# Performance work log

Measured on AMD Instinct MI355X. Metric: run time of the kernel, lower is better.

Reference implementation:

```python
import jax, jax.numpy as jnp
import numpy as np

B, S, D, H = 128, 1024, 512, 512


def setup_inputs() -> dict:
    key = jax.random.key(0)
    ks = jax.random.split(key, 8)
    return {
        "input": jax.random.normal(ks[0], (B, D), jnp.float32),
        "context": jax.random.normal(ks[1], (B, S, D), jnp.float32),
        "mask": jax.random.randint(ks[2], (B, S), 0, 2).astype(bool),
        "W_in": jax.random.normal(ks[3], (H, D), jnp.float32) * (1.0 / np.sqrt(D)),
        "b_in": jax.random.normal(ks[4], (H,), jnp.float32) * 0.01,
        "W_ctx": jax.random.normal(ks[5], (H, D), jnp.float32) * (1.0 / np.sqrt(D)),
        "b_ctx": jax.random.normal(ks[6], (H,), jnp.float32) * 0.01,
        "V": jax.random.uniform(ks[7], (H,), jnp.float32, -1.0, 1.0),
    }


def reference(input, context, mask, W_in, b_in, W_ctx, b_ctx, V):
    # inp: [B, H] -> broadcast over S (torch: unsqueeze(2).expand)
    inp = input @ W_in.T + b_in
    # 1x1 Conv1d over permuted context == per-position linear: [B, H, S]
    ctx = jnp.einsum('bsd,hd->bhs', context, W_ctx) + b_ctx[None, :, None]
    # additive (Bahdanau) score: V . tanh(inp + ctx) over H -> [B, S]
    att = jnp.einsum('h,bhs->bs', V, jnp.tanh(inp[:, :, None] + ctx))
    att = jnp.where(mask, -jnp.inf, att)
    alpha = jax.nn.softmax(att, axis=-1)  # [B, S]
    # weighted sum of projected context: [B, H]
    hidden_state = jnp.einsum('bhs,bs->bh', ctx, alpha)
    return (hidden_state, alpha)
```

## Files before the change

### kernel.cpp

```cpp
#include <hip/hip_runtime.h>
#include <math.h>

#define B_ 128
#define S_ 1024
#define D_ 512
#define H_ 512

typedef _Float16 f16x4 __attribute__((ext_vector_type(4)));
typedef _Float16 f16x8 __attribute__((ext_vector_type(8)));
typedef float    f32x4 __attribute__((ext_vector_type(4)));

__global__ void zero_k(float* __restrict__ p, int n) {
    int i = blockIdx.x * 256 + threadIdx.x;
    if (i < n) p[i] = 0.f;
}

__global__ __launch_bounds__(256) void linear_k(const float* __restrict__ X,
                                                const float* __restrict__ W,
                                                const float* __restrict__ bias,
                                                float* __restrict__ out) {
    int idx = blockIdx.x * 256 + threadIdx.x;
    int b = idx >> 9;
    int h = idx & 511;
    const float4* x = (const float4*)(X + (size_t)b * D_);
    const float4* w = (const float4*)(W + (size_t)h * D_);
    float s = 0.f;
#pragma unroll 8
    for (int k = 0; k < D_ / 4; ++k) {
        float4 xv = x[k], wv = w[k];
        s = fmaf(xv.x, wv.x, s);
        s = fmaf(xv.y, wv.y, s);
        s = fmaf(xv.z, wv.z, s);
        s = fmaf(xv.w, wv.w, s);
    }
    out[idx] = s + bias[h];
}

__device__ inline f16x4 cvt4(float4 v) {
    f16x4 r;
    r[0] = (_Float16)v.x; r[1] = (_Float16)v.y;
    r[2] = (_Float16)v.z; r[3] = (_Float16)v.w;
    return r;
}

__device__ inline float fast_tanh(float x) {
    float e = __expf(2.f * x);
    return 1.f - 2.f / (e + 1.f);
}

__global__ __launch_bounds__(256) void score_mfma(const float* __restrict__ ctx,
                                                  const float* __restrict__ Wc,
                                                  const float* __restrict__ bc,
                                                  const float* __restrict__ Vv,
                                                  const float* __restrict__ inp,
                                                  float* __restrict__ att) {
    __shared__ __align__(16) _Float16 Ah[128][40];
    __shared__ __align__(16) _Float16 Bh[128][40];
    __shared__ float red[8][128];

    const int tid = threadIdx.x;
    const int h0 = blockIdx.x * 128;
    const int s0 = blockIdx.y * 128;
    const int b  = blockIdx.z;

    const int rb  = tid >> 3;
    const int grp = tid & 7;

    const int wave = tid >> 6;
    const int lane = tid & 63;
    const int wm = wave >> 1, wn = wave & 1;
    const int l15 = lane & 15, quad = lane >> 4;

    const float* Abase = Wc  + (size_t)(h0 + rb) * D_ + grp * 4;
    const float* Bbase = ctx + ((size_t)b * S_ + s0 + rb) * D_ + grp * 4;

    f32x4 acc[4][4];
#pragma unroll
    for (int mi = 0; mi < 4; ++mi)
#pragma unroll
        for (int ni = 0; ni < 4; ++ni) acc[mi][ni] = (f32x4){0.f, 0.f, 0.f, 0.f};

    float4 ra[4], rbv[4];
#pragma unroll
    for (int i = 0; i < 4; ++i) {
        ra[i]  = *(const float4*)(Abase + (size_t)(32 * i) * D_);
        rbv[i] = *(const float4*)(Bbase + (size_t)(32 * i) * D_);
    }

    for (int k0 = 0; k0 < D_; k0 += 32) {
        __syncthreads();
#pragma unroll
        for (int i = 0; i < 4; ++i) {
            const int row = rb + 32 * i;
            *(f16x4*)&Ah[row][grp * 4] = cvt4(ra[i]);
            *(f16x4*)&Bh[row][grp * 4] = cvt4(rbv[i]);
        }
        __syncthreads();
        if (k0 + 32 < D_) {
#pragma unroll
            for (int i = 0; i < 4; ++i) {
                ra[i]  = *(const float4*)(Abase + (size_t)(32 * i) * D_ + k0 + 32);
                rbv[i] = *(const float4*)(Bbase + (size_t)(32 * i) * D_ + k0 + 32);
            }
        }
        f16x8 bhf[4];
#pragma unroll
        for (int ni = 0; ni < 4; ++ni)
            bhf[ni] = *(const f16x8*)&Bh[wn * 64 + ni * 16 + l15][quad * 8];
#pragma unroll
        for (int mi = 0; mi < 4; ++mi) {
            f16x8 ah = *(const f16x8*)&Ah[wm * 64 + mi * 16 + l15][quad * 8];
#pragma unroll
            for (int ni = 0; ni < 4; ++ni)
                acc[mi][ni] = __builtin_amdgcn_mfma_f32_16x16x32_f16(ah, bhf[ni], acc[mi][ni], 0, 0, 0);
        }
    }

    float p[4] = {0.f, 0.f, 0.f, 0.f};
#pragma unroll
    for (int mi = 0; mi < 4; ++mi) {
#pragma unroll
        for (int r = 0; r < 4; ++r) {
            const int h = h0 + wm * 64 + mi * 16 + quad * 4 + r;
            const float c  = inp[(size_t)b * H_ + h] + bc[h];
            const float vh = Vv[h];
#pragma unroll
            for (int ni = 0; ni < 4; ++ni)
                p[ni] = fmaf(vh, fast_tanh(c + acc[mi][ni][r]), p[ni]);
        }
    }
    const int cid = wm * 4 + quad;
#pragma unroll
    for (int ni = 0; ni < 4; ++ni)
        red[cid][wn * 64 + ni * 16 + l15] = p[ni];
    __syncthreads();
    if (tid < 128) {
        float s = 0.f;
#pragma unroll
        for (int g = 0; g < 8; ++g) s += red[g][tid];
        atomicAdd(att + (size_t)b * S_ + s0 + tid, s);
    }
}

__global__ __launch_bounds__(256) void softmax_k(const float* __restrict__ att,
                                                 const int* __restrict__ mask,
                                                 float* __restrict__ alpha) {
    const int b = blockIdx.x;
    const int t = threadIdx.x;
    __shared__ float sm[256];
    float v[4];
    float mx = -INFINITY;
#pragma unroll
    for (int i = 0; i < 4; ++i) {
        int s = t + i * 256;
        float a = att[(size_t)b * S_ + s];
        int mk = mask[(size_t)b * S_ + s];
        v[i] = mk ? -INFINITY : a;
        mx = fmaxf(mx, v[i]);
    }
    sm[t] = mx;
    __syncthreads();
    for (int off = 128; off > 0; off >>= 1) {
        if (t < off) sm[t] = fmaxf(sm[t], sm[t + off]);
        __syncthreads();
    }
    mx = sm[0];
    __syncthreads();
    float e[4];
    float sum = 0.f;
#pragma unroll
    for (int i = 0; i < 4; ++i) {
        e[i] = expf(v[i] - mx);
        sum += e[i];
    }
    sm[t] = sum;
    __syncthreads();
    for (int off = 128; off > 0; off >>= 1) {
        if (t < off) sm[t] += sm[t + off];
        __syncthreads();
    }
    float inv = 1.f / sm[0];
#pragma unroll
    for (int i = 0; i < 4; ++i) alpha[(size_t)b * S_ + t + i * 256] = e[i] * inv;
}

__global__ __launch_bounds__(256) void cbar_k(const float* __restrict__ ctx,
                                              const float* __restrict__ alpha,
                                              float* __restrict__ cbar) {
    const int b = blockIdx.y;
    const int s0 = blockIdx.x * 128;
    const int t = threadIdx.x;
    const int c4 = t & 127;
    const int sh = t >> 7;
    __shared__ float al[128];
    __shared__ float4 red[128];
    if (t < 128) al[t] = alpha[(size_t)b * S_ + s0 + t];
    __syncthreads();
    const float4* base = (const float4*)(ctx + ((size_t)b * S_ + s0) * D_);
    float4 c = {0.f, 0.f, 0.f, 0.f};
#pragma unroll 4
    for (int s = sh; s < 128; s += 2) {
        float a = al[s];
        float4 x = base[(size_t)s * (D_ / 4) + c4];
        c.x = fmaf(a, x.x, c.x);
        c.y = fmaf(a, x.y, c.y);
        c.z = fmaf(a, x.z, c.z);
        c.w = fmaf(a, x.w, c.w);
    }
    if (sh == 1) red[c4] = c;
    __syncthreads();
    if (sh == 0) {
        float4 o = red[c4];
        float* dst = cbar + (size_t)b * D_ + c4 * 4;
        atomicAdd(dst + 0, c.x + o.x);
        atomicAdd(dst + 1, c.y + o.y);
        atomicAdd(dst + 2, c.z + o.z);
        atomicAdd(dst + 3, c.w + o.w);
    }
}

extern "C" void kernel_launch(void* const* d_in, const int* in_sizes, int n_in,
                              void* d_out, int out_size, void* d_ws, size_t ws_size,
                              hipStream_t stream) {
    const float* input = (const float*)d_in[0];
    const float* ctx   = (const float*)d_in[1];
    const int*   mask  = (const int*)d_in[2];
    const float* W_in  = (const float*)d_in[3];
    const float* b_in  = (const float*)d_in[4];
    const float* W_ctx = (const float*)d_in[5];
    const float* b_ctx = (const float*)d_in[6];
    const float* V     = (const float*)d_in[7];

    float* hidden = (float*)d_out;
    float* alpha  = (float*)d_out + B_ * H_;

    float* inp  = (float*)d_ws;
    float* att  = inp + B_ * H_;
    float* cbar = att + B_ * S_;

    int nz = B_ * S_ + B_ * D_;
    zero_k<<<(nz + 255) / 256, 256, 0, stream>>>(att, nz);

    linear_k<<<(B_ * H_) / 256, 256, 0, stream>>>(input, W_in, b_in, inp);

    dim3 g2(H_ / 128, S_ / 128, B_);
    score_mfma<<<g2, 256, 0, stream>>>(ctx, W_ctx, b_ctx, V, inp, att);

    softmax_k<<<B_, 256, 0, stream>>>(att, mask, alpha);

    dim3 g4(S_ / 128, B_);
    cbar_k<<<g4, 256, 0, stream>>>(ctx, alpha, cbar);

    linear_k<<<(B_ * H_) / 256, 256, 0, stream>>>(cbar, W_ctx, b_ctx, hidden);
}
```

Baseline: 586.8 us.

## Async-copy context tiles into swizzled LDS and preconvert W_ctx to fp16

```diff
diff --git a/kernel.cpp b/kernel.cpp
--- a/kernel.cpp
+++ b/kernel.cpp
@@ -10,9 +10,30 @@
 typedef _Float16 f16x8 __attribute__((ext_vector_type(8)));
 typedef float    f32x4 __attribute__((ext_vector_type(4)));
 
+typedef __attribute__((address_space(3))) uint32_t lds_u32_t;
+typedef const __attribute__((address_space(1))) uint32_t glb_u32_t;
+
+__device__ __forceinline__ void async_copy16(const void* gsrc, void* ldst) {
+    __builtin_amdgcn_global_load_lds((glb_u32_t*)gsrc, (lds_u32_t*)ldst, 16, 0, 0);
+}
+
 __global__ void zero_k(float* __restrict__ p, int n) {
     int i = blockIdx.x * 256 + threadIdx.x;
     if (i < n) p[i] = 0.f;
+}
+
+__device__ inline f16x4 cvt4(float4 v) {
+    f16x4 r;
+    r[0] = (_Float16)v.x; r[1] = (_Float16)v.y;
+    r[2] = (_Float16)v.z; r[3] = (_Float16)v.w;
+    return r;
+}
+
+__global__ __launch_bounds__(256) void w16_k(const float* __restrict__ W,
+                                             _Float16* __restrict__ out) {
+    int i = blockIdx.x * 256 + threadIdx.x;
+    float4 v = ((const float4*)W)[i];
+    *(f16x4*)(out + 4 * (size_t)i) = cvt4(v);
 }
 
 __global__ __launch_bounds__(256) void linear_k(const float* __restrict__ X,
@@ -36,43 +57,38 @@
     out[idx] = s + bias[h];
 }
 
-__device__ inline f16x4 cvt4(float4 v) {
-    f16x4 r;
-    r[0] = (_Float16)v.x; r[1] = (_Float16)v.y;
-    r[2] = (_Float16)v.z; r[3] = (_Float16)v.w;
-    return r;
-}
-
 __device__ inline float fast_tanh(float x) {
     float e = __expf(2.f * x);
     return 1.f - 2.f / (e + 1.f);
 }
 
 __global__ __launch_bounds__(256) void score_mfma(const float* __restrict__ ctx,
-                                                  const float* __restrict__ Wc,
+                                                  const _Float16* __restrict__ W16,
                                                   const float* __restrict__ bc,
                                                   const float* __restrict__ Vv,
                                                   const float* __restrict__ inp,
                                                   float* __restrict__ att) {
-    __shared__ __align__(16) _Float16 Ah[128][40];
-    __shared__ __align__(16) _Float16 Bh[128][40];
+    __shared__ __align__(16) float Bs[2][4096];
     __shared__ float red[8][128];
 
     const int tid = threadIdx.x;
-    const int h0 = blockIdx.x * 128;
-    const int s0 = blockIdx.y * 128;
-    const int b  = blockIdx.z;
-
-    const int rb  = tid >> 3;
-    const int grp = tid & 7;
+    const int f   = blockIdx.x;
+    const int xcd = f & 7;
+    const int hb  = (f >> 3) & 3;
+    const int g   = (f >> 5) * 8 + xcd;
+    const int h0  = hb * 128;
+    const int s0  = (g & 7) * 128;
+    const int b   = g >> 3;
 
     const int wave = tid >> 6;
     const int lane = tid & 63;
     const int wm = wave >> 1, wn = wave & 1;
     const int l15 = lane & 15, quad = lane >> 4;
 
-    const float* Abase = Wc  + (size_t)(h0 + rb) * D_ + grp * 4;
-    const float* Bbase = ctx + ((size_t)b * S_ + s0 + rb) * D_ + grp * 4;
+    const int lrow  = lane >> 3;
+    const int lslot = lane & 7;
+    const int gk    = lslot ^ lrow;
+    const float* bsrc = ctx + ((size_t)b * S_ + s0 + 32 * wave + lrow) * D_ + gk * 4;
 
     f32x4 acc[4][4];
 #pragma unroll
@@ -80,40 +96,52 @@
 #pragma unroll
         for (int ni = 0; ni < 4; ++ni) acc[mi][ni] = (f32x4){0.f, 0.f, 0.f, 0.f};
 
-    float4 ra[4], rbv[4];
-#pragma unroll
-    for (int i = 0; i < 4; ++i) {
-        ra[i]  = *(const float4*)(Abase + (size_t)(32 * i) * D_);
-        rbv[i] = *(const float4*)(Bbase + (size_t)(32 * i) * D_);
-    }
-
-    for (int k0 = 0; k0 < D_; k0 += 32) {
+    const _Float16* Afrag = W16 + (size_t)(h0 + wm * 64 + l15) * D_ + quad * 8;
+
+#pragma unroll
+    for (int it = 0; it < 4; ++it)
+        async_copy16(bsrc + (size_t)it * 8 * D_, &Bs[0][wave * 1024 + it * 256]);
+    f16x8 af[4], afn[4];
+#pragma unroll
+    for (int mi = 0; mi < 4; ++mi)
+        af[mi] = *(const f16x8*)(Afrag + (size_t)mi * 16 * D_);
+    __syncthreads();
+
+    for (int ks = 0; ks < 16; ++ks) {
+        const int buf = ks & 1;
+        if (ks < 15) {
+            const float* sb = bsrc + (ks + 1) * 32;
+#pragma unroll
+            for (int it = 0; it < 4; ++it)
+                async_copy16(sb + (size_t)it * 8 * D_, &Bs[buf ^ 1][wave * 1024 + it * 256]);
+#pragma unroll
+            for (int mi = 0; mi < 4; ++mi)
+                afn[mi] = *(const f16x8*)(Afrag + (size_t)mi * 16 * D_ + (ks + 1) * 32);
+        }
+        f16x8 bf[4];
+#pragma unroll
+        for (int ni = 0; ni < 4; ++ni) {
+            const int r = wn * 64 + ni * 16 + l15;
+            const int rr = r & 7;
+            const int base = (r >> 3) * 256 + rr * 32;
+            const int s1 = (2 * quad) ^ rr;
+            f32x4 u = *(const f32x4*)&Bs[buf][base + s1 * 4];
+            f32x4 v = *(const f32x4*)&Bs[buf][base + (s1 ^ 1) * 4];
+            f16x8 h;
+            h[0] = (_Float16)u[0]; h[1] = (_Float16)u[1];
+            h[2] = (_Float16)u[2]; h[3] = (_Float16)u[3];
+            h[4] = (_Float16)v[0]; h[5] = (_Float16)v[1];
+            h[6] = (_Float16)v[2]; h[7] = (_Float16)v[3];
+            bf[ni] = h;
+        }
+#pragma unroll
+        for (int mi = 0; mi < 4; ++mi)
+#pragma unroll
+            for (int ni = 0; ni < 4; ++ni)
+                acc[mi][ni] = __builtin_amdgcn_mfma_f32_16x16x32_f16(af[mi], bf[ni], acc[mi][ni], 0, 0, 0);
+#pragma unroll
+        for (int mi = 0; mi < 4; ++mi) af[mi] = afn[mi];
         __syncthreads();
-#pragma unroll
-        for (int i = 0; i < 4; ++i) {
-            const int row = rb + 32 * i;
-            *(f16x4*)&Ah[row][grp * 4] = cvt4(ra[i]);
-            *(f16x4*)&Bh[row][grp * 4] = cvt4(rbv[i]);
-        }
-        __syncthreads();
-        if (k0 + 32 < D_) {
-#pragma unroll
-            for (int i = 0; i < 4; ++i) {
-                ra[i]  = *(const float4*)(Abase + (size_t)(32 * i) * D_ + k0 + 32);
-                rbv[i] = *(const float4*)(Bbase + (size_t)(32 * i) * D_ + k0 + 32);
-            }
-        }
-        f16x8 bhf[4];
-#pragma unroll
-        for (int ni = 0; ni < 4; ++ni)
-            bhf[ni] = *(const f16x8*)&Bh[wn * 64 + ni * 16 + l15][quad * 8];
-#pragma unroll
-        for (int mi = 0; mi < 4; ++mi) {
-            f16x8 ah = *(const f16x8*)&Ah[wm * 64 + mi * 16 + l15][quad * 8];
-#pragma unroll
-            for (int ni = 0; ni < 4; ++ni)
-                acc[mi][ni] = __builtin_amdgcn_mfma_f32_16x16x32_f16(ah, bhf[ni], acc[mi][ni], 0, 0, 0);
-        }
     }
 
     float p[4] = {0.f, 0.f, 0.f, 0.f};
@@ -137,7 +165,7 @@
     if (tid < 128) {
         float s = 0.f;
 #pragma unroll
-        for (int g = 0; g < 8; ++g) s += red[g][tid];
+        for (int gg = 0; gg < 8; ++gg) s += red[gg][tid];
         atomicAdd(att + (size_t)b * S_ + s0 + tid, s);
     }
 }
@@ -237,14 +265,16 @@
     float* inp  = (float*)d_ws;
     float* att  = inp + B_ * H_;
     float* cbar = att + B_ * S_;
+    _Float16* W16 = (_Float16*)(cbar + B_ * D_);
 
     int nz = B_ * S_ + B_ * D_;
     zero_k<<<(nz + 255) / 256, 256, 0, stream>>>(att, nz);
 
+    w16_k<<<(H_ * D_ / 4) / 256, 256, 0, stream>>>(W_ctx, W16);
+
     linear_k<<<(B_ * H_) / 256, 256, 0, stream>>>(input, W_in, b_in, inp);
 
-    dim3 g2(H_ / 128, S_ / 128, B_);
-    score_mfma<<<g2, 256, 0, stream>>>(ctx, W_ctx, b_ctx, V, inp, att);
+    score_mfma<<<4096, 256, 0, stream>>>(ctx, W16, b_ctx, V, inp, att);
 
     softmax_k<<<B_, 256, 0, stream>>>(att, mask, alpha);
 
```

Result: slower. 605.9 us (+3.3%).

## Pre-convert context and weights to fp16 and pipeline the score GEMM with async LDS loads

Applied to the files above, without the earlier changes.

```diff
diff --git a/kernel.cpp b/kernel.cpp
--- a/kernel.cpp
+++ b/kernel.cpp
@@ -10,9 +10,61 @@
 typedef _Float16 f16x8 __attribute__((ext_vector_type(8)));
 typedef float    f32x4 __attribute__((ext_vector_type(4)));
 
+typedef __attribute__((address_space(3))) uint32_t lds_u32_t;
+typedef const __attribute__((address_space(1))) uint32_t glb_u32_t;
+
+__device__ __forceinline__ void async_copy16(const void* gsrc, void* ldst) {
+    __builtin_amdgcn_global_load_lds((glb_u32_t*)gsrc, (lds_u32_t*)ldst, 16, 0, 0);
+}
+
 __global__ void zero_k(float* __restrict__ p, int n) {
     int i = blockIdx.x * 256 + threadIdx.x;
     if (i < n) p[i] = 0.f;
+}
+
+__device__ inline f16x4 cvt4(float4 v) {
+    f16x4 r;
+    r[0] = (_Float16)v.x; r[1] = (_Float16)v.y;
+    r[2] = (_Float16)v.z; r[3] = (_Float16)v.w;
+    return r;
+}
+
+__device__ inline float fast_tanh(float x) {
+    float e = __expf(2.f * x);
+    return 1.f - 2.f / (e + 1.f);
+}
+
+__global__ __launch_bounds__(256) void prep_k(const float* __restrict__ ctx,
+                                              const float* __restrict__ W,
+                                              _Float16* __restrict__ ctx16,
+                                              _Float16* __restrict__ W16,
+                                              float* __restrict__ zp) {
+    const int bid = blockIdx.x;
+    const int t = threadIdx.x;
+    if (bid < 32768) {
+        size_t i = (size_t)bid * 256 + t;
+        const float4* src = (const float4*)ctx;
+        float4 a = src[2 * i], b = src[2 * i + 1];
+        f16x8 o;
+        o[0] = (_Float16)a.x; o[1] = (_Float16)a.y;
+        o[2] = (_Float16)a.z; o[3] = (_Float16)a.w;
+        o[4] = (_Float16)b.x; o[5] = (_Float16)b.y;
+        o[6] = (_Float16)b.z; o[7] = (_Float16)b.w;
+        *(f16x8*)(ctx16 + i * 8) = o;
+    } else if (bid < 32768 + 128) {
+        size_t i = (size_t)(bid - 32768) * 256 + t;
+        const float4* src = (const float4*)W;
+        float4 a = src[2 * i], b = src[2 * i + 1];
+        f16x8 o;
+        o[0] = (_Float16)a.x; o[1] = (_Float16)a.y;
+        o[2] = (_Float16)a.z; o[3] = (_Float16)a.w;
+        o[4] = (_Float16)b.x; o[5] = (_Float16)b.y;
+        o[6] = (_Float16)b.z; o[7] = (_Float16)b.w;
+        *(f16x8*)(W16 + i * 8) = o;
+    } else {
+        int i = (bid - 32896) * 256 + t;
+        ((float4*)zp)[i] = (float4){0.f, 0.f, 0.f, 0.f};
+    }
 }
 
 __global__ __launch_bounds__(256) void linear_k(const float* __restrict__ X,
@@ -36,43 +88,33 @@
     out[idx] = s + bias[h];
 }
 
-__device__ inline f16x4 cvt4(float4 v) {
-    f16x4 r;
-    r[0] = (_Float16)v.x; r[1] = (_Float16)v.y;
-    r[2] = (_Float16)v.z; r[3] = (_Float16)v.w;
-    return r;
-}
-
-__device__ inline float fast_tanh(float x) {
-    float e = __expf(2.f * x);
-    return 1.f - 2.f / (e + 1.f);
-}
-
-__global__ __launch_bounds__(256) void score_mfma(const float* __restrict__ ctx,
-                                                  const float* __restrict__ Wc,
-                                                  const float* __restrict__ bc,
-                                                  const float* __restrict__ Vv,
-                                                  const float* __restrict__ inp,
-                                                  float* __restrict__ att) {
-    __shared__ __align__(16) _Float16 Ah[128][40];
-    __shared__ __align__(16) _Float16 Bh[128][40];
+__global__ __launch_bounds__(256) void score_f16(const _Float16* __restrict__ ctx16,
+                                                 const _Float16* __restrict__ W16,
+                                                 const float* __restrict__ bc,
+                                                 const float* __restrict__ Vv,
+                                                 const float* __restrict__ inp,
+                                                 float* __restrict__ att) {
+    __shared__ __align__(16) _Float16 Bs[2][8192];
     __shared__ float red[8][128];
 
     const int tid = threadIdx.x;
-    const int h0 = blockIdx.x * 128;
-    const int s0 = blockIdx.y * 128;
-    const int b  = blockIdx.z;
-
-    const int rb  = tid >> 3;
-    const int grp = tid & 7;
+    const int f   = blockIdx.x;
+    const int xcd = f & 7;
+    const int hb  = (f >> 3) & 3;
+    const int g   = (f >> 5) * 8 + xcd;
+    const int h0  = hb * 128;
+    const int s0  = (g & 7) * 128;
+    const int b   = g >> 3;
 
     const int wave = tid >> 6;
     const int lane = tid & 63;
     const int wm = wave >> 1, wn = wave & 1;
     const int l15 = lane & 15, quad = lane >> 4;
 
-    const float* Abase = Wc  + (size_t)(h0 + rb) * D_ + grp * 4;
-    const float* Bbase = ctx + ((size_t)b * S_ + s0 + rb) * D_ + grp * 4;
+    const int lrow  = lane >> 3;
+    const int lslot = lane & 7;
+    const int gk    = lslot ^ lrow;
+    const _Float16* bsrc = ctx16 + ((size_t)b * S_ + s0 + 32 * wave + lrow) * D_ + gk * 8;
 
     f32x4 acc[4][4];
 #pragma unroll
@@ -80,40 +122,55 @@
 #pragma unroll
         for (int ni = 0; ni < 4; ++ni) acc[mi][ni] = (f32x4){0.f, 0.f, 0.f, 0.f};
 
-    float4 ra[4], rbv[4];
-#pragma unroll
-    for (int i = 0; i < 4; ++i) {
-        ra[i]  = *(const float4*)(Abase + (size_t)(32 * i) * D_);
-        rbv[i] = *(const float4*)(Bbase + (size_t)(32 * i) * D_);
-    }
-
-    for (int k0 = 0; k0 < D_; k0 += 32) {
+    const _Float16* Afrag = W16 + (size_t)(h0 + wm * 64 + l15) * D_ + quad * 8;
+
+#pragma unroll
+    for (int it = 0; it < 4; ++it)
+        async_copy16(bsrc + (size_t)it * 8 * D_, &Bs[0][(wave * 32 + it * 8) * 64]);
+    f16x8 af[4][2], afn[4][2];
+#pragma unroll
+    for (int mi = 0; mi < 4; ++mi)
+#pragma unroll
+        for (int kh = 0; kh < 2; ++kh)
+            af[mi][kh] = *(const f16x8*)(Afrag + (size_t)mi * 16 * D_ + kh * 32);
+    __syncthreads();
+
+    for (int ks = 0; ks < 8; ++ks) {
+        const int buf = ks & 1;
+        if (ks < 7) {
+            const _Float16* sb = bsrc + (ks + 1) * 64;
+#pragma unroll
+            for (int it = 0; it < 4; ++it)
+                async_copy16(sb + (size_t)it * 8 * D_, &Bs[buf ^ 1][(wave * 32 + it * 8) * 64]);
+#pragma unroll
+            for (int mi = 0; mi < 4; ++mi)
+#pragma unroll
+                for (int kh = 0; kh < 2; ++kh)
+                    afn[mi][kh] = *(const f16x8*)(Afrag + (size_t)mi * 16 * D_ + (ks + 1) * 64 + kh * 32);
+        }
+        f16x8 bf[4][2];
+#pragma unroll
+        for (int ni = 0; ni < 4; ++ni) {
+            const int r = wn * 64 + ni * 16 + l15;
+            const int rr = r & 7;
+#pragma unroll
+            for (int kh = 0; kh < 2; ++kh) {
+                const int slot = (kh * 4 + quad) ^ rr;
+                bf[ni][kh] = *(const f16x8*)&Bs[buf][r * 64 + slot * 8];
+            }
+        }
+#pragma unroll
+        for (int kh = 0; kh < 2; ++kh)
+#pragma unroll
+            for (int mi = 0; mi < 4; ++mi)
+#pragma unroll
+                for (int ni = 0; ni < 4; ++ni)
+                    acc[mi][ni] = __builtin_amdgcn_mfma_f32_16x16x32_f16(af[mi][kh], bf[ni][kh], acc[mi][ni], 0, 0, 0);
+#pragma unroll
+        for (int mi = 0; mi < 4; ++mi)
+#pragma unroll
+            for (int kh = 0; kh < 2; ++kh) af[mi][kh] = afn[mi][kh];
         __syncthreads();
-#pragma unroll
-        for (int i = 0; i < 4; ++i) {
-            const int row = rb + 32 * i;
-            *(f16x4*)&Ah[row][grp * 4] = cvt4(ra[i]);
-            *(f16x4*)&Bh[row][grp * 4] = cvt4(rbv[i]);
-        }
-        __syncthreads();
-        if (k0 + 32 < D_) {
-#pragma unroll
-            for (int i = 0; i < 4; ++i) {
-                ra[i]  = *(const float4*)(Abase + (size_t)(32 * i) * D_ + k0 + 32);
-                rbv[i] = *(const float4*)(Bbase + (size_t)(32 * i) * D_ + k0 + 32);
-            }
-        }
-        f16x8 bhf[4];
-#pragma unroll
-        for (int ni = 0; ni < 4; ++ni)
-            bhf[ni] = *(const f16x8*)&Bh[wn * 64 + ni * 16 + l15][quad * 8];
-#pragma unroll
-        for (int mi = 0; mi < 4; ++mi) {
-            f16x8 ah = *(const f16x8*)&Ah[wm * 64 + mi * 16 + l15][quad * 8];
-#pragma unroll
-            for (int ni = 0; ni < 4; ++ni)
-                acc[mi][ni] = __builtin_amdgcn_mfma_f32_16x16x32_f16(ah, bhf[ni], acc[mi][ni], 0, 0, 0);
-        }
     }
 
     float p[4] = {0.f, 0.f, 0.f, 0.f};
@@ -137,7 +194,7 @@
     if (tid < 128) {
         float s = 0.f;
 #pragma unroll
-        for (int g = 0; g < 8; ++g) s += red[g][tid];
+        for (int gg = 0; gg < 8; ++gg) s += red[gg][tid];
         atomicAdd(att + (size_t)b * S_ + s0 + tid, s);
     }
 }
@@ -184,9 +241,133 @@
     for (int i = 0; i < 4; ++i) alpha[(size_t)b * S_ + t + i * 256] = e[i] * inv;
 }
 
-__global__ __launch_bounds__(256) void cbar_k(const float* __restrict__ ctx,
-                                              const float* __restrict__ alpha,
-                                              float* __restrict__ cbar) {
+__global__ __launch_bounds__(256) void cbar16_k(const _Float16* __restrict__ ctx16,
+                                                const float* __restrict__ alpha,
+                                                float* __restrict__ cbar) {
+    const int b = blockIdx.y;
+    const int s0 = blockIdx.x * 128;
+    const int t = threadIdx.x;
+    const int c8 = t & 63;
+    const int sh = t >> 6;
+    __shared__ float al[128];
+    __shared__ float red[3][512];
+    if (t < 128) al[t] = alpha[(size_t)b * S_ + s0 + t];
+    __syncthreads();
+    const f16x8* base = (const f16x8*)(ctx16 + ((size_t)b * S_ + s0) * D_);
+    float acc[8] = {0.f, 0.f, 0.f, 0.f, 0.f, 0.f, 0.f, 0.f};
+#pragma unroll 4
+    for (int s = sh; s < 128; s += 4) {
+        float a = al[s];
+        f16x8 x = base[(size_t)s * 64 + c8];
+#pragma unroll
+        for (int j = 0; j < 8; ++j) acc[j] = fmaf(a, (float)x[j], acc[j]);
+    }
+    if (sh > 0) {
+#pragma unroll
+        for (int j = 0; j < 8; ++j) red[sh - 1][c8 * 8 + j] = acc[j];
+    }
+    __syncthreads();
+    if (sh == 0) {
+        float* dst = cbar + (size_t)b * D_ + c8 * 8;
+#pragma unroll
+        for (int j = 0; j < 8; ++j)
+            atomicAdd(dst + j, acc[j] + red[0][c8 * 8 + j] + red[1][c8 * 8 + j] + red[2][c8 * 8 + j]);
+    }
+}
+
+__global__ __launch_bounds__(256) void score_v3(const float* __restrict__ ctx,
+                                                const float* __restrict__ Wc,
+                                                const float* __restrict__ bc,
+                                                const float* __restrict__ Vv,
+                                                const float* __restrict__ inp,
+                                                float* __restrict__ att) {
+    __shared__ __align__(16) _Float16 Ah[128][40];
+    __shared__ __align__(16) _Float16 Bh[128][40];
+    __shared__ float red[8][128];
+
+    const int tid = threadIdx.x;
+    const int h0 = blockIdx.x * 128;
+    const int s0 = blockIdx.y * 128;
+    const int b  = blockIdx.z;
+    const int rb  = tid >> 3;
+    const int grp = tid & 7;
+    const int wave = tid >> 6;
+    const int lane = tid & 63;
+    const int wm = wave >> 1, wn = wave & 1;
+    const int l15 = lane & 15, quad = lane >> 4;
+
+    const float* Abase = Wc  + (size_t)(h0 + rb) * D_ + grp * 4;
+    const float* Bbase = ctx + ((size_t)b * S_ + s0 + rb) * D_ + grp * 4;
+
+    f32x4 acc[4][4];
+#pragma unroll
+    for (int mi = 0; mi < 4; ++mi)
+#pragma unroll
+        for (int ni = 0; ni < 4; ++ni) acc[mi][ni] = (f32x4){0.f, 0.f, 0.f, 0.f};
+
+    float4 ra[4], rbv[4];
+#pragma unroll
+    for (int i = 0; i < 4; ++i) {
+        ra[i]  = *(const float4*)(Abase + (size_t)(32 * i) * D_);
+        rbv[i] = *(const float4*)(Bbase + (size_t)(32 * i) * D_);
+    }
+    for (int k0 = 0; k0 < D_; k0 += 32) {
+        __syncthreads();
+#pragma unroll
+        for (int i = 0; i < 4; ++i) {
+            const int row = rb + 32 * i;
+            *(f16x4*)&Ah[row][grp * 4] = cvt4(ra[i]);
+            *(f16x4*)&Bh[row][grp * 4] = cvt4(rbv[i]);
+        }
+        __syncthreads();
+        if (k0 + 32 < D_) {
+#pragma unroll
+            for (int i = 0; i < 4; ++i) {
+                ra[i]  = *(const float4*)(Abase + (size_t)(32 * i) * D_ + k0 + 32);
+                rbv[i] = *(const float4*)(Bbase + (size_t)(32 * i) * D_ + k0 + 32);
+            }
+        }
+        f16x8 bhf[4];
+#pragma unroll
+        for (int ni = 0; ni < 4; ++ni)
+            bhf[ni] = *(const f16x8*)&Bh[wn * 64 + ni * 16 + l15][quad * 8];
+#pragma unroll
+        for (int mi = 0; mi < 4; ++mi) {
+            f16x8 ah = *(const f16x8*)&Ah[wm * 64 + mi * 16 + l15][quad * 8];
+#pragma unroll
+            for (int ni = 0; ni < 4; ++ni)
+                acc[mi][ni] = __builtin_amdgcn_mfma_f32_16x16x32_f16(ah, bhf[ni], acc[mi][ni], 0, 0, 0);
+        }
+    }
+    float p[4] = {0.f, 0.f, 0.f, 0.f};
+#pragma unroll
+    for (int mi = 0; mi < 4; ++mi) {
+#pragma unroll
+        for (int r = 0; r < 4; ++r) {
+            const int h = h0 + wm * 64 + mi * 16 + quad * 4 + r;
+            const float c  = inp[(size_t)b * H_ + h] + bc[h];
+            const float vh = Vv[h];
+#pragma unroll
+            for (int ni = 0; ni < 4; ++ni)
+                p[ni] = fmaf(vh, fast_tanh(c + acc[mi][ni][r]), p[ni]);
+        }
+    }
+    const int cid = wm * 4 + quad;
+#pragma unroll
+    for (int ni = 0; ni < 4; ++ni)
+        red[cid][wn * 64 + ni * 16 + l15] = p[ni];
+    __syncthreads();
+    if (tid < 128) {
+        float s = 0.f;
+#pragma unroll
+        for (int gg = 0; gg < 8; ++gg) s += red[gg][tid];
+        atomicAdd(att + (size_t)b * S_ + s0 + tid, s);
+    }
+}
+
+__global__ __launch_bounds__(256) void cbar32_k(const float* __restrict__ ctx,
+                                                const float* __restrict__ alpha,
+                                                float* __restrict__ cbar) {
     const int b = blockIdx.y;
     const int s0 = blockIdx.x * 128;
     const int t = threadIdx.x;
@@ -238,18 +419,29 @@
     float* att  = inp + B_ * H_;
     float* cbar = att + B_ * S_;
 
-    int nz = B_ * S_ + B_ * D_;
-    zero_k<<<(nz + 255) / 256, 256, 0, stream>>>(att, nz);
-
-    linear_k<<<(B_ * H_) / 256, 256, 0, stream>>>(input, W_in, b_in, inp);
-
-    dim3 g2(H_ / 128, S_ / 128, B_);
-    score_mfma<<<g2, 256, 0, stream>>>(ctx, W_ctx, b_ctx, V, inp, att);
-
-    softmax_k<<<B_, 256, 0, stream>>>(att, mask, alpha);
-
-    dim3 g4(S_ / 128, B_);
-    cbar_k<<<g4, 256, 0, stream>>>(ctx, alpha, cbar);
-
-    linear_k<<<(B_ * H_) / 256, 256, 0, stream>>>(cbar, W_ctx, b_ctx, hidden);
-}
+    const size_t need = (size_t)(B_ * H_ + B_ * S_ + B_ * D_) * 4
+                      + (size_t)H_ * D_ * 2 + (size_t)B_ * S_ * D_ * 2;
+
+    if (ws_size >= need) {
+        _Float16* W16   = (_Float16*)(cbar + B_ * D_);
+        _Float16* ctx16 = W16 + (size_t)H_ * D_;
+
+        prep_k<<<33088, 256, 0, stream>>>(ctx, W_ctx, ctx16, W16, att);
+        linear_k<<<(B_ * H_) / 256, 256, 0, stream>>>(input, W_in, b_in, inp);
+        score_f16<<<4096, 256, 0, stream>>>(ctx16, W16, b_ctx, V, inp, att);
+        softmax_k<<<B_, 256, 0, stream>>>(att, mask, alpha);
+        dim3 g4(S_ / 128, B_);
+        cbar16_k<<<g4, 256, 0, stream>>>(ctx16, alpha, cbar);
+        linear_k<<<(B_ * H_) / 256, 256, 0, stream>>>(cbar, W_ctx, b_ctx, hidden);
+    } else {
+        int nz = B_ * S_ + B_ * D_;
+        zero_k<<<(nz + 255) / 256, 256, 0, stream>>>(att, nz);
+        linear_k<<<(B_ * H_) / 256, 256, 0, stream>>>(input, W_in, b_in, inp);
+        dim3 g2(H_ / 128, S_ / 128, B_);
+        score_v3<<<g2, 256, 0, stream>>>(ctx, W_ctx, b_ctx, V, inp, att);
+        softmax_k<<<B_, 256, 0, stream>>>(att, mask, alpha);
+        dim3 g4(S_ / 128, B_);
+        cbar32_k<<<g4, 256, 0, stream>>>(ctx, alpha, cbar);
+        linear_k<<<(B_ * H_) / 256, 256, 0, stream>>>(cbar, W_ctx, b_ctx, hidden);
+    }
+}
```

After: 628.7 us. +7.1%, slower.
